# Optimization experiments

Measured on AMD Instinct MI355X. Metric: run time of the kernel, lower is better.

## Reference

```python
import jax, jax.numpy as jnp
import numpy as np

B, C, N = 4, 128, 8192
CQK = C // 4  # query/key projection dim = out_channels // 4


def setup_inputs() -> dict:
    key = jax.random.key(0)
    ks = jax.random.split(key, 9)
    s_in = 1.0 / np.sqrt(C)
    return {
        "x": jax.random.normal(ks[0], (B, C, N), dtype=jnp.float32),
        "xyz": jax.random.normal(ks[1], (B, N, 3), dtype=jnp.float32),
        "Wq": jax.random.normal(ks[2], (CQK, C), dtype=jnp.float32) * s_in,
        "bq": jax.random.normal(ks[3], (CQK,), dtype=jnp.float32) * 0.01,
        "Wk": jax.random.normal(ks[4], (CQK, C), dtype=jnp.float32) * s_in,
        "bk": jax.random.normal(ks[5], (CQK,), dtype=jnp.float32) * 0.01,
        "Wv": jax.random.normal(ks[6], (C, C), dtype=jnp.float32) * s_in,
        "bv": jax.random.normal(ks[7], (C,), dtype=jnp.float32) * 0.01,
        "gamma": jax.random.normal(ks[8], (1,), dtype=jnp.float32) * 0.1,
    }


def reference(x, xyz, Wq, bq, Wk, bk, Wv, bv, gamma):
    # 1x1 Conv1d == per-point linear projection over channels
    q = jnp.einsum('oc,bcn->bon', Wq, x) + bq[None, :, None]   # (B, CQK, N)
    k = jnp.einsum('oc,bcn->bon', Wk, x) + bk[None, :, None]   # (B, CQK, N)
    v = jnp.einsum('oc,bcn->bon', Wv, x) + bv[None, :, None]   # (B, C, N)

    # energy[b, n, m] = <q[:, n], k[:, m]>
    energy = jnp.einsum('bcn,bcm->bnm', q, k)                  # (B, N, N)

    # positional correlation bias: normalize coords per point, cosine-sim matrix
    xyz_bcn = jnp.swapaxes(xyz, 1, 2)                          # (B, 3, N)
    xyz_norm = xyz_bcn / (jnp.linalg.norm(xyz_bcn, axis=1, keepdims=True) + 1e-8)
    pos_corr = jnp.einsum('bcn,bcm->bnm', xyz_norm, xyz_norm)  # (B, N, N)
    energy = energy + 0.1 * pos_corr

    attention = jax.nn.softmax(energy, axis=-1)                # rowwise over m

    # out[b, c, n] = sum_m v[b, c, m] * attention[b, n, m]
    out = jnp.einsum('bcm,bnm->bcn', v, attention)             # (B, C, N)
    return gamma * out + x
```

## Files before the change

kernel.cpp:

```cpp
#include <hip/hip_runtime.h>

#define NPTS 8192
#define NB 4
#define NCH 128
#define DQK 48
#define TK 64
#define SPLIT 4
#define KEYS_PER (NPTS / SPLIT)
#define ROUNDS (KEYS_PER / TK)
#define SH2 28.853901f
#define LOG2E 1.4426950408889634f

typedef unsigned short ushort_t;
typedef unsigned int uint_t;
typedef __attribute__((ext_vector_type(8))) short bf16x8;
typedef __attribute__((ext_vector_type(4))) float f32x4;
typedef __attribute__((ext_vector_type(16))) float f32x16;

static __device__ __forceinline__ ushort_t f2bf(float x) {
  union { float f; uint_t u; } v; v.f = x;
  uint_t r = v.u + 0x7fffu + ((v.u >> 16) & 1u);
  return (ushort_t)(r >> 16);
}
static __device__ __forceinline__ float bf2f(ushort_t u) {
  union { uint_t i; float f; } v; v.i = ((uint_t)u) << 16; return v.f;
}
static __device__ __forceinline__ int sig16(int n) {
  int g2 = (n >> 2) & 3;
  return (g2 == 1 || g2 == 2) ? (n ^ 0xC) : n;
}

typedef __attribute__((address_space(1))) void void_g;
typedef __attribute__((address_space(3))) void void_l;
static __device__ __forceinline__ void gload_lds16(const ushort_t* g, ushort_t* l) {
  __builtin_amdgcn_global_load_lds((void_g*)(ushort_t*)g, (void_l*)l, 16, 0, 0);
}

__global__ __launch_bounds__(512, 1)
void wprep_kernel(const float* __restrict__ Wq, const float* __restrict__ bq,
                  const float* __restrict__ Wk, const float* __restrict__ bk,
                  const float* __restrict__ Wv, const float* __restrict__ bv,
                  ushort_t* __restrict__ Wb, float* __restrict__ bias_pre) {
  const int z = blockIdx.x;
  const int ks = threadIdx.x >> 6;
  const int lane = threadIdx.x & 63;
  const int l31 = lane & 31, h = lane >> 5;
  const float* W = (z == 0) ? Wq : (z == 1) ? Wk : (Wv + (size_t)(z - 2) * 32 * 128);
  const float sc = (z == 0) ? LOG2E : 1.0f;
  const float* wr = W + l31 * 128 + ks * 16 + h * 8;
  union { ushort_t u[8]; bf16x8 v; } p;
#pragma unroll
  for (int j = 0; j < 8; ++j) p.u[j] = f2bf(wr[j] * sc);
  *(bf16x8*)(Wb + ((size_t)(z * 8 + ks) * 64 + lane) * 8) = p.v;
  if (z == 0 && threadIdx.x < 192) {
    int i = threadIdx.x;
    bias_pre[i] = (i < 32) ? bq[i] * LOG2E : (i < 64) ? bk[i - 32] : bv[i - 64];
  }
}

__global__ __launch_bounds__(256, 4)
void projm2_kernel(const float* __restrict__ x, const float* __restrict__ xyz,
                   const ushort_t* __restrict__ Wb,
                   const float* __restrict__ bias_pre,
                   ushort_t* __restrict__ Qb, ushort_t* __restrict__ Kb,
                   ushort_t* __restrict__ Vt) {
  const int tid = threadIdx.x;
  const int lane = tid & 63, wv = tid >> 6;
  const int l31 = lane & 31, h = lane >> 5;
  const int b = blockIdx.y;
  const int n = blockIdx.x * 128 + wv * 32 + l31;

  bf16x8 bfr[8];
  const float* xb = x + (size_t)b * NCH * NPTS + n;
#pragma unroll
  for (int ks = 0; ks < 8; ++ks) {
    const float* xc = xb + (size_t)(ks * 16 + h * 8) * NPTS;
    union { ushort_t u[8]; bf16x8 v; } p;
#pragma unroll
    for (int j = 0; j < 8; ++j) p.u[j] = f2bf(xc[(size_t)j * NPTS]);
    bfr[ks] = p.v;
  }

  float xa = xyz[((size_t)b * NPTS + n) * 3 + 0];
  float xc2 = xyz[((size_t)b * NPTS + n) * 3 + 1];
  float xd = xyz[((size_t)b * NPTS + n) * 3 + 2];
  float rinv = 1.0f / (sqrtf(xa * xa + xc2 * xc2 + xd * xd) + 1e-8f);

#pragma unroll 1
  for (int z = 0; z < 6; ++z) {
    f32x16 S;
#pragma unroll
    for (int r = 0; r < 16; ++r)
      S[r] = bias_pre[z * 32 + (r & 3) + 8 * (r >> 2) + 4 * h];
#pragma unroll
    for (int ks = 0; ks < 8; ++ks) {
      bf16x8 af = *(const bf16x8*)(Wb + ((size_t)(z * 8 + ks) * 64 + lane) * 8);
      S = __builtin_amdgcn_mfma_f32_32x32x16_bf16(af, bfr[ks], S, 0, 0, 0);
    }
    if (z <= 1) {
      float sc = (z == 0) ? LOG2E : 1.0f;
      ushort_t* dst = (z == 0 ? Qb : Kb) + ((size_t)b * NPTS + n) * DQK;
#pragma unroll
      for (int r = 0; r < 16; ++r)
        dst[(r & 3) + 8 * (r >> 2) + 4 * h] = f2bf(S[r]);
      float rn = 0.31622776601683794f * sc * rinv;
      union { ushort_t u[16]; bf16x8 v[2]; } t;
#pragma unroll
      for (int j = 0; j < 16; ++j) t.u[j] = 0;
      t.u[0] = f2bf(xa * rn); t.u[1] = f2bf(xc2 * rn); t.u[2] = f2bf(xd * rn);
      t.u[3] = (z == 0) ? f2bf(-SH2) : f2bf(1.0f);
      *(bf16x8*)(dst + 32) = t.v[0];
      *(bf16x8*)(dst + 40) = t.v[1];
    } else {
      const int np = (n & ~15) | sig16(n & 15);
      const int c0 = (z - 2) * 32;
#pragma unroll
      for (int r = 0; r < 16; ++r)
        Vt[((size_t)b * NCH + c0 + (r & 3) + 8 * (r >> 2) + 4 * h) * NPTS + np] =
            f2bf(S[r]);
    }
  }
}

__global__ __launch_bounds__(512, 4)
void attn32_kernel(const ushort_t* __restrict__ Qb, const ushort_t* __restrict__ Kb,
                   const ushort_t* __restrict__ Vt,
                   ushort_t* __restrict__ PACC, float* __restrict__ PL) {
  __shared__ __align__(16) ushort_t L[2][16][512];
  const int tid = threadIdx.x;
  const int lane = tid & 63, w = tid >> 6;
  const int l31 = lane & 31, h = lane >> 5;

  const int lin = blockIdx.x;
  const int bs = lin & 15;
  const int b = bs & 3, sseg = bs >> 2;
  const int qblk = lin >> 4;
  const int q0w = qblk * 256 + w * 32;
  const int m00 = sseg * KEYS_PER;

  bf16x8 qf[3];
#pragma unroll
  for (int c = 0; c < 3; ++c)
    qf[c] = *(const bf16x8*)(Qb + ((size_t)b * NPTS + q0w + l31) * DQK +
                             c * 16 + h * 8);

  const ushort_t* gp[2];
  int fid[2];
#pragma unroll
  for (int i = 0; i < 2; ++i) {
    int fi = w * 2 + i;
    fid[i] = fi;
    int fch = fi >> 2, kk = fi & 3;
    gp[i] = Vt + ((size_t)b * NCH + fch * 32 + l31) * NPTS + m00 + kk * 16 + h * 8;
  }

  const ushort_t* kp = Kb + ((size_t)b * NPTS + m00 + l31) * DQK + h * 8;

  f32x16 O[4];
#pragma unroll
  for (int f = 0; f < 4; ++f) O[f] = (f32x16)(0.f);
  float ls0 = 0.f, ls1 = 0.f;

#pragma unroll
  for (int i = 0; i < 2; ++i) gload_lds16(gp[i], &L[0][fid[i]][0]);

#pragma unroll 1
  for (int t = 0; t < ROUNDS; ++t) {
    __syncthreads();
    const int cur = t & 1;
    if (t + 1 < ROUNDS) {
#pragma unroll
      for (int i = 0; i < 2; ++i) {
        gp[i] += TK;
        gload_lds16(gp[i], &L[cur ^ 1][fid[i]][0]);
      }
    }

#pragma unroll
    for (int kb = 0; kb < 2; ++kb) {
      const ushort_t* kpb = kp + (size_t)kb * 32 * DQK;
      bf16x8 kf0 = *(const bf16x8*)(kpb);
      bf16x8 kf1 = *(const bf16x8*)(kpb + 16);
      bf16x8 kf2 = *(const bf16x8*)(kpb + 32);

      __builtin_amdgcn_s_setprio(1);
      f32x16 S = __builtin_amdgcn_mfma_f32_32x32x16_bf16(kf0, qf[0],
                                                         (f32x16)(0.f), 0, 0, 0);
      S = __builtin_amdgcn_mfma_f32_32x32x16_bf16(kf1, qf[1], S, 0, 0, 0);
      S = __builtin_amdgcn_mfma_f32_32x32x16_bf16(kf2, qf[2], S, 0, 0, 0);
      __builtin_amdgcn_s_setprio(0);

      uint_t pk[8];
#pragma unroll
      for (int i = 0; i < 8; ++i) {
        float p0 = __builtin_amdgcn_exp2f(S[2 * i]);
        float p1 = __builtin_amdgcn_exp2f(S[2 * i + 1]);
        ls0 += p0;
        ls1 += p1;
        pk[i] = __builtin_amdgcn_perm(__float_as_uint(p1), __float_as_uint(p0),
                                      0x07060302u);
      }

#pragma unroll
      for (int kkl = 0; kkl < 2; ++kkl) {
        union { uint_t u[4]; bf16x8 v; } au;
        au.u[0] = pk[4 * kkl + 0];
        au.u[1] = pk[4 * kkl + 1];
        au.u[2] = pk[4 * kkl + 2];
        au.u[3] = pk[4 * kkl + 3];
        bf16x8 A = au.v;
        __builtin_amdgcn_s_setprio(1);
#pragma unroll
        for (int f = 0; f < 4; ++f) {
          bf16x8 vf = *(const bf16x8*)(&L[cur][f * 4 + kb * 2 + kkl][0] + lane * 8);
          O[f] = __builtin_amdgcn_mfma_f32_32x32x16_bf16(A, vf, O[f], 0, 0, 0);
        }
        __builtin_amdgcn_s_setprio(0);
      }
    }
    kp += (size_t)TK * DQK;
  }

  float lsum = ls0 + ls1;
  lsum += __shfl_xor(lsum, 32);
  const size_t pbase = (size_t)(bs * 16 + (qblk >> 1)) * 16 + (qblk & 1) * 8 + w;
#pragma unroll
  for (int f = 0; f < 4; ++f) {
    union { ushort_t u[16]; bf16x8 v[2]; } pu;
#pragma unroll
    for (int r = 0; r < 16; ++r) pu.u[r] = f2bf(O[f][r]);
    size_t idx = (pbase * 4 + f) * 1024 + (size_t)lane * 16;
    *(bf16x8*)(PACC + idx) = pu.v[0];
    *(bf16x8*)(PACC + idx + 8) = pu.v[1];
  }
  if (lane < 32) PL[(size_t)bs * NPTS + q0w + lane] = lsum;
}

#define MPITCH 268
__global__ __launch_bounds__(256, 4)
void merge4c_kernel(const ushort_t* __restrict__ PACC, const float* __restrict__ PL,
                    const float* __restrict__ x, const float* __restrict__ gamma,
                    float* __restrict__ out) {
  __shared__ float Linv[256];
  __shared__ float ldso[32 * MPITCH];
  const int tid = threadIdx.x;
  const int qblk2 = blockIdx.x, b = blockIdx.y, f = blockIdx.z;
  const int q0 = qblk2 * 256;

  float Ls = 0.f;
#pragma unroll
  for (int s = 0; s < 4; ++s)
    Ls += PL[(size_t)(s * 4 + b) * NPTS + q0 + tid];
  Linv[tid] = gamma[0] / Ls;
  __syncthreads();

  const int ww = tid >> 6, lane = tid & 63, l31 = lane & 31, h = lane >> 5;

#pragma unroll
  for (int g = 0; g < 2; ++g) {
    float acc[16];
#pragma unroll
    for (int r = 0; r < 16; ++r) acc[r] = 0.f;
#pragma unroll
    for (int s = 0; s < 4; ++s) {
      size_t idx = (((((size_t)(s * 4 + b) * 16 + (qblk2 >> 1)) * 8 +
                      (qblk2 & 1) * 4 + ww) * 2 + g) * 4 + f) * 1024 +
                   (size_t)lane * 16;
      bf16x8 a0 = *(const bf16x8*)(PACC + idx);
      bf16x8 a1 = *(const bf16x8*)(PACC + idx + 8);
#pragma unroll
      for (int r = 0; r < 8; ++r) {
        acc[r] += bf2f((ushort_t)a0[r]);
        acc[8 + r] += bf2f((ushort_t)a1[r]);
      }
    }
    const int qb = ww * 64 + g * 32 + 4 * h;
#pragma unroll
    for (int rr = 0; rr < 4; ++rr) {
      int q = qb + 8 * rr;
      f32x4 v;
#pragma unroll
      for (int i = 0; i < 4; ++i) v[i] = acc[rr * 4 + i] * Linv[q + i];
      *(f32x4*)&ldso[l31 * MPITCH + q] = v;
    }
  }
  __syncthreads();

  const float* xb = x + ((size_t)b * NCH + f * 32) * NPTS + q0;
  float* ob = out + ((size_t)b * NCH + f * 32) * NPTS + q0;
#pragma unroll
  for (int rr = 0; rr < 8; ++rr) {
    int ch = ww * 8 + rr;
    f32x4 v = *(const f32x4*)&ldso[ch * MPITCH + lane * 4];
    f32x4 xv = *(const f32x4*)(xb + (size_t)ch * NPTS + lane * 4);
    v += xv;
    *(f32x4*)(ob + (size_t)ch * NPTS + lane * 4) = v;
  }
}

extern "C" void kernel_launch(void* const* d_in, const int* in_sizes, int n_in,
                              void* d_out, int out_size, void* d_ws,
                              size_t ws_size, hipStream_t stream) {
  const float* x     = (const float*)d_in[0];
  const float* xyz   = (const float*)d_in[1];
  const float* Wq    = (const float*)d_in[2];
  const float* bq    = (const float*)d_in[3];
  const float* Wk    = (const float*)d_in[4];
  const float* bk    = (const float*)d_in[5];
  const float* Wv    = (const float*)d_in[6];
  const float* bv    = (const float*)d_in[7];
  const float* gamma = (const float*)d_in[8];
  float* out = (float*)d_out;

  const size_t BN = (size_t)NB * NPTS;
  ushort_t* Qb = (ushort_t*)d_ws;
  ushort_t* Kb = Qb + BN * DQK;
  ushort_t* Vt = Kb + BN * DQK;
  ushort_t* PACC = Vt + BN * NCH;
  float* PL = (float*)(PACC + (size_t)16 * 16 * 8 * 2 * 4 * 1024);
  ushort_t* Wb = (ushort_t*)(PL + 16 * BN / 2);
  float* bias_pre = (float*)(Wb + 6 * 8 * 64 * 8);

  wprep_kernel<<<6, 512, 0, stream>>>(Wq, bq, Wk, bk, Wv, bv, Wb, bias_pre);
  projm2_kernel<<<dim3(NPTS / 128, NB), 256, 0, stream>>>(
      x, xyz, Wb, bias_pre, Qb, Kb, Vt);
  attn32_kernel<<<512, 512, 0, stream>>>(Qb, Kb, Vt, PACC, PL);
  merge4c_kernel<<<dim3(32, NB, 4), 256, 0, stream>>>(PACC, PL, x, gamma, out);
  (void)in_sizes; (void)n_in; (void)out_size; (void)ws_size;
}
```

Before: 197.6 us.

## Store Q, K, V in MFMA-fragment-native tiled layouts for contiguous lane loads

The projection kernel now writes Q and K in per-32-point tiles laid out as MFMA operand fragments (512 elements per k-chunk), and V in 64-key tiles matching the LDS fragment order. The attention kernel reads each fragment with one fully contiguous 16-byte-per-lane load instead of strided 96-byte-row accesses. The first K block's loads are also issued before the V prefetch to start them earlier. This trades scattered 2-byte stores in the projection kernel for coalesced reads in the hot attention loop.

```diff
diff --git a/kernel.cpp b/kernel.cpp
--- a/kernel.cpp
+++ b/kernel.cpp
@@ -35,6 +35,7 @@
 static __device__ __forceinline__ void gload_lds16(const ushort_t* g, ushort_t* l) {
   __builtin_amdgcn_global_load_lds((void_g*)(ushort_t*)g, (void_l*)l, 16, 0, 0);
 }
+
 
 __global__ __launch_bounds__(512, 1)
 void wprep_kernel(const float* __restrict__ Wq, const float* __restrict__ bq,
@@ -98,26 +99,33 @@
       S = __builtin_amdgcn_mfma_f32_32x32x16_bf16(af, bfr[ks], S, 0, 0, 0);
     }
     if (z <= 1) {
+      ushort_t* dstf = (z == 0 ? Qb : Kb) +
+                       (((size_t)b * 256 + (n >> 5)) * 3) * 512;
+      const int lbase = l31 * 8;
+#pragma unroll
+      for (int r = 0; r < 16; ++r) {
+        int idx = (r >> 3) * 512 + ((r >> 2) & 1) * 256 + lbase + (r & 3) + 4 * h;
+        dstf[idx] = f2bf(S[r]);
+      }
       float sc = (z == 0) ? LOG2E : 1.0f;
-      ushort_t* dst = (z == 0 ? Qb : Kb) + ((size_t)b * NPTS + n) * DQK;
-#pragma unroll
-      for (int r = 0; r < 16; ++r)
-        dst[(r & 3) + 8 * (r >> 2) + 4 * h] = f2bf(S[r]);
       float rn = 0.31622776601683794f * sc * rinv;
       union { ushort_t u[16]; bf16x8 v[2]; } t;
 #pragma unroll
       for (int j = 0; j < 16; ++j) t.u[j] = 0;
       t.u[0] = f2bf(xa * rn); t.u[1] = f2bf(xc2 * rn); t.u[2] = f2bf(xd * rn);
       t.u[3] = (z == 0) ? f2bf(-SH2) : f2bf(1.0f);
-      *(bf16x8*)(dst + 32) = t.v[0];
-      *(bf16x8*)(dst + 40) = t.v[1];
+      *(bf16x8*)(dstf + 1024 + lbase) = t.v[0];
+      *(bf16x8*)(dstf + 1024 + 256 + lbase) = t.v[1];
     } else {
       const int np = (n & ~15) | sig16(n & 15);
-      const int c0 = (z - 2) * 32;
-#pragma unroll
-      for (int r = 0; r < 16; ++r)
-        Vt[((size_t)b * NCH + c0 + (r & 3) + 8 * (r >> 2) + 4 * h) * NPTS + np] =
-            f2bf(S[r]);
+      const size_t base =
+          (((size_t)b * 128 + (np >> 6)) * 16 + (z - 2) * 4 + ((np >> 4) & 3)) * 512 +
+          ((np >> 3) & 1) * 256 + (np & 7);
+#pragma unroll
+      for (int r = 0; r < 16; ++r) {
+        int dd = (r & 3) + 8 * (r >> 2) + 4 * h;
+        Vt[base + dd * 8] = f2bf(S[r]);
+      }
     }
   }
 }
@@ -129,7 +137,7 @@
   __shared__ __align__(16) ushort_t L[2][16][512];
   const int tid = threadIdx.x;
   const int lane = tid & 63, w = tid >> 6;
-  const int l31 = lane & 31, h = lane >> 5;
+  const int l31 = lane & 31;
 
   const int lin = blockIdx.x;
   const int bs = lin & 15;
@@ -139,49 +147,49 @@
   const int m00 = sseg * KEYS_PER;
 
   bf16x8 qf[3];
-#pragma unroll
-  for (int c = 0; c < 3; ++c)
-    qf[c] = *(const bf16x8*)(Qb + ((size_t)b * NPTS + q0w + l31) * DQK +
-                             c * 16 + h * 8);
-
-  const ushort_t* gp[2];
-  int fid[2];
-#pragma unroll
-  for (int i = 0; i < 2; ++i) {
-    int fi = w * 2 + i;
-    fid[i] = fi;
-    int fch = fi >> 2, kk = fi & 3;
-    gp[i] = Vt + ((size_t)b * NCH + fch * 32 + l31) * NPTS + m00 + kk * 16 + h * 8;
-  }
-
-  const ushort_t* kp = Kb + ((size_t)b * NPTS + m00 + l31) * DQK + h * 8;
+  {
+    const ushort_t* qbase = Qb + (((size_t)b * 256 + (q0w >> 5)) * 3) * 512 + lane * 8;
+#pragma unroll
+    for (int c = 0; c < 3; ++c) qf[c] = *(const bf16x8*)(qbase + c * 512);
+  }
+
+  const ushort_t* kbase = Kb + (((size_t)b * 256 + (m00 >> 5)) * 3) * 512 + lane * 8;
+  const ushort_t* vsrc = Vt + (((size_t)b * 128 + (m00 >> 6)) * 16) * 512 + lane * 8;
+  const int f0 = 2 * w, f1 = 2 * w + 1;
 
   f32x16 O[4];
 #pragma unroll
   for (int f = 0; f < 4; ++f) O[f] = (f32x16)(0.f);
   float ls0 = 0.f, ls1 = 0.f;
 
-#pragma unroll
-  for (int i = 0; i < 2; ++i) gload_lds16(gp[i], &L[0][fid[i]][0]);
+  gload_lds16(vsrc + f0 * 512, &L[0][f0][0]);
+  gload_lds16(vsrc + f1 * 512, &L[0][f1][0]);
 
 #pragma unroll 1
   for (int t = 0; t < ROUNDS; ++t) {
     __syncthreads();
     const int cur = t & 1;
+
+    bf16x8 ka0 = *(const bf16x8*)(kbase);
+    bf16x8 ka1 = *(const bf16x8*)(kbase + 512);
+    bf16x8 ka2 = *(const bf16x8*)(kbase + 1024);
+
     if (t + 1 < ROUNDS) {
-#pragma unroll
-      for (int i = 0; i < 2; ++i) {
-        gp[i] += TK;
-        gload_lds16(gp[i], &L[cur ^ 1][fid[i]][0]);
-      }
+      vsrc += 16 * 512;
+      gload_lds16(vsrc + f0 * 512, &L[cur ^ 1][f0][0]);
+      gload_lds16(vsrc + f1 * 512, &L[cur ^ 1][f1][0]);
     }
 
 #pragma unroll
     for (int kb = 0; kb < 2; ++kb) {
-      const ushort_t* kpb = kp + (size_t)kb * 32 * DQK;
-      bf16x8 kf0 = *(const bf16x8*)(kpb);
-      bf16x8 kf1 = *(const bf16x8*)(kpb + 16);
-      bf16x8 kf2 = *(const bf16x8*)(kpb + 32);
+      bf16x8 kf0, kf1, kf2;
+      if (kb == 0) {
+        kf0 = ka0; kf1 = ka1; kf2 = ka2;
+      } else {
+        kf0 = *(const bf16x8*)(kbase + 1536);
+        kf1 = *(const bf16x8*)(kbase + 2048);
+        kf2 = *(const bf16x8*)(kbase + 2560);
+      }
 
       __builtin_amdgcn_s_setprio(1);
       f32x16 S = __builtin_amdgcn_mfma_f32_32x32x16_bf16(kf0, qf[0],
@@ -218,7 +226,7 @@
         __builtin_amdgcn_s_setprio(0);
       }
     }
-    kp += (size_t)TK * DQK;
+    kbase += 3072;
   }
 
   float lsum = ls0 + ls1;
```

Result: faster. 193.2 us (-2.2%).
